# Optimization experiments

Hardware: AMD Instinct MI355X
Metric: run time of the kernel (lower is better)

Reference implementation:

```python
import jax, jax.numpy as jnp
import numpy as np

EMBED_DIM = 384


def setup_inputs() -> dict:
    key = jax.random.key(0)
    k1, k2, k3 = jax.random.split(key, 3)
    B, P, N, C = 32, 4, 1024, EMBED_DIM
    x = jax.random.normal(k1, (B, P, N, C), dtype=jnp.float32)
    # 1x1 Conv2D on channel-last == linear on last dim; kernel [Cin, Cout]
    w_qkv = jax.random.normal(k2, (C, 1 + 2 * C), dtype=jnp.float32) * (1.0 / np.sqrt(C))
    b_qkv = jnp.zeros((1 + 2 * C,), dtype=jnp.float32)
    w_proj = jax.random.normal(k3, (C, C), dtype=jnp.float32) * (1.0 / np.sqrt(C))
    b_proj = jnp.zeros((C,), dtype=jnp.float32)
    return {"x": x, "w_qkv": w_qkv, "b_qkv": b_qkv, "w_proj": w_proj, "b_proj": b_proj}


def reference(x, w_qkv, b_qkv, w_proj, b_proj):
    C = EMBED_DIM
    # qkv pointwise conv: [B,P,N,C] @ [C, 1+2C]
    qkv = jnp.einsum('bpnc,cd->bpnd', x, w_qkv) + b_qkv
    query = qkv[..., :1]                 # [B,P,N,1]
    key_t = qkv[..., 1:1 + C]            # [B,P,N,C]
    value = qkv[..., 1 + C:]             # [B,P,N,C]
    # NOTE: softmax over the trailing axis of size 1 (faithful to source) -> all ones
    context_scores = jax.nn.softmax(query, axis=-1)
    # key * scores, reduce-sum over patch-index axis (axis=2), keepdims
    context_vector = jnp.sum(key_t * context_scores, axis=2, keepdims=True)  # [B,P,1,C]
    gated = jax.nn.relu(value) * context_vector                              # [B,P,N,C]
    out = jnp.einsum('bpnc,cd->bpnd', gated, w_proj) + b_proj
    return out
```

## Files before the change

kernel.cpp:

```cpp
#include <hip/hip_runtime.h>
#include <hip/hip_bf16.h>
#include <type_traits>
#include <utility>

#define C_    384
#define N_    1024
#define G_    128
#define QKVD  769

typedef float  f32x4 __attribute__((ext_vector_type(4)));
typedef short  s16x8 __attribute__((ext_vector_type(8)));
typedef __bf16 b16x8 __attribute__((ext_vector_type(8)));

template <typename V, typename = void>
struct mfma_takes : std::false_type {};
template <typename V>
struct mfma_takes<V, std::void_t<decltype(__builtin_amdgcn_mfma_f32_16x16x32_bf16(
    std::declval<V>(), std::declval<V>(), std::declval<f32x4>(), 0, 0, 0))>>
    : std::true_type {};

using frag_t = std::conditional_t<mfma_takes<s16x8>::value, s16x8, b16x8>;

template <typename V>
__device__ __forceinline__ f32x4 mfma_bf16(V a, V b, f32x4 c) {
  return __builtin_amdgcn_mfma_f32_16x16x32_bf16(a, b, c, 0, 0, 0);
}

__device__ __forceinline__ unsigned short f2bf(float f) {
  union { float f; unsigned u; } v; v.f = f;
  unsigned r = v.u + 0x7fffu + ((v.u >> 16) & 1u);
  return (unsigned short)(r >> 16);
}
__device__ __forceinline__ unsigned pack2(float lo, float hi) {
  return (unsigned)f2bf(lo) | ((unsigned)f2bf(hi) << 16);
}

__global__ __launch_bounds__(384) void k_xsum(const float* __restrict__ x,
                                              float* __restrict__ xsum) {
  __shared__ float sh[4][C_];
  const int tid = threadIdx.x;
  const int c4  = (tid % 96) * 4;
  const int rg  = tid / 96;
  const int b   = blockIdx.x;
  const int g   = b >> 3;
  const float* p = x + ((size_t)b * 128 + (size_t)rg * 32) * C_ + c4;
  f32x4 s = {0.f, 0.f, 0.f, 0.f};
#pragma unroll 8
  for (int r = 0; r < 32; ++r) {
    float4 v = *(const float4*)(p + (size_t)r * C_);
    s.x += v.x; s.y += v.y; s.z += v.z; s.w += v.w;
  }
  *(f32x4*)&sh[rg][c4] = s;
  __syncthreads();
  if (rg == 0) {
#pragma unroll
    for (int j = 0; j < 4; ++j) {
      float v = sh[0][c4 + j] + sh[1][c4 + j] + sh[2][c4 + j] + sh[3][c4 + j];
      atomicAdd(&xsum[g * C_ + c4 + j], v);
    }
  }
}

__global__ void k_cv(const float* __restrict__ xsum, const float* __restrict__ w_qkv,
                     const float* __restrict__ b_qkv, float* __restrict__ cv) {
  __shared__ float xs[C_];
  int g = blockIdx.x, c = threadIdx.x;
  xs[c] = xsum[g * C_ + c];
  __syncthreads();
  float acc = 0.f;
#pragma unroll 4
  for (int k = 0; k < C_; ++k) acc += xs[k] * w_qkv[k * QKVD + 1 + c];
  cv[g * C_ + c] = acc + (float)N_ * b_qkv[1 + c];
}

__global__ void k_pack(const float* __restrict__ w_qkv, const float* __restrict__ w_proj,
                       unsigned short* __restrict__ pWv, unsigned short* __restrict__ pWp) {
  int bid = blockIdx.x;
  int mat = bid / 288;
  int r   = bid % 288;
  int kk = r / 24, nf = r % 24;
  int lane = threadIdx.x;
  int kbase = kk * 32 + (lane >> 4) * 8;
  int n = nf * 16 + (lane & 15);
  unsigned v[4];
#pragma unroll
  for (int jj = 0; jj < 4; ++jj) {
    int k0 = kbase + jj * 2;
    float f0 = mat ? w_proj[(size_t)k0 * C_ + n]       : w_qkv[(size_t)k0 * QKVD + 385 + n];
    float f1 = mat ? w_proj[(size_t)(k0 + 1) * C_ + n] : w_qkv[(size_t)(k0 + 1) * QKVD + 385 + n];
    v[jj] = (unsigned)f2bf(f0) | ((unsigned)f2bf(f1) << 16);
  }
  unsigned short* dst = (mat ? pWp : pWv) + ((size_t)r * 64 + lane) * 8;
  uint4 w; w.x = v[0]; w.y = v[1]; w.z = v[2]; w.w = v[3];
  *(uint4*)dst = w;
}

__global__ __launch_bounds__(256) void k_fused(
    const float* __restrict__ x, const unsigned short* __restrict__ pWv,
    const unsigned short* __restrict__ pWp, const float* __restrict__ cv,
    const float* __restrict__ b_qkv, const float* __restrict__ b_proj,
    float* __restrict__ out) {
  __shared__ __align__(16) char tile[32 * 768];
  __shared__ float cv_l[C_], bv_l[C_], bp_l[C_];

  const int tid  = threadIdx.x;
  const int lane = tid & 63;
  const int wv   = tid >> 6;
  const int R0   = blockIdx.x * 32;
  const int g    = R0 >> 10;

  for (int c = tid; c < C_; c += 256) {
    cv_l[c] = cv[g * C_ + c];
    bv_l[c] = b_qkv[1 + C_ + c];
    bp_l[c] = b_proj[c];
  }

  {
    const float* xg = x + (size_t)R0 * C_;
#pragma unroll
    for (int j = 0; j < 6; ++j) {
      int ch  = tid + j * 256;
      int row = ch / 48;
      int c8  = (ch % 48) * 8;
      const float4* s0 = (const float4*)(xg + (size_t)row * C_ + c8);
      float4 a = s0[0], b = s0[1];
      uint4 w;
      w.x = pack2(a.x, a.y); w.y = pack2(a.z, a.w);
      w.z = pack2(b.x, b.y); w.w = pack2(b.z, b.w);
      int byte = (row * 768 + c8 * 2) ^ ((row & 7) << 4);
      *(uint4*)(tile + byte) = w;
    }
  }
  __syncthreads();

  const f32x4 zero = {0.f, 0.f, 0.f, 0.f};
  f32x4 acc[2][6];
#pragma unroll
  for (int m = 0; m < 2; ++m)
#pragma unroll
    for (int n = 0; n < 6; ++n) acc[m][n] = zero;

  for (int kk = 0; kk < 12; ++kk) {
    frag_t A[2], Bv[6];
    int kb2 = (kk * 32 + (lane >> 4) * 8) * 2;
#pragma unroll
    for (int m = 0; m < 2; ++m) {
      int row = m * 16 + (lane & 15);
      A[m] = *(const frag_t*)(tile + ((row * 768 + kb2) ^ ((row & 7) << 4)));
    }
    const unsigned short* bp_ = pWv + ((size_t)(kk * 24 + wv * 6) * 64 + lane) * 8;
#pragma unroll
    for (int n = 0; n < 6; ++n) Bv[n] = *(const frag_t*)(bp_ + (size_t)n * 64 * 8);
#pragma unroll
    for (int m = 0; m < 2; ++m)
#pragma unroll
      for (int n = 0; n < 6; ++n) acc[m][n] = mfma_bf16(A[m], Bv[n], acc[m][n]);
  }
  __syncthreads();

#pragma unroll
  for (int m = 0; m < 2; ++m) {
#pragma unroll
    for (int n = 0; n < 6; ++n) {
      int col = wv * 96 + n * 16 + (lane & 15);
      float cvv = cv_l[col], bvv = bv_l[col];
#pragma unroll
      for (int r = 0; r < 4; ++r) {
        int row = m * 16 + (lane >> 4) * 4 + r;
        float val = fmaxf(acc[m][n][r] + bvv, 0.f) * cvv;
        *(unsigned short*)(tile + ((row * 768 + col * 2) ^ ((row & 7) << 4))) = f2bf(val);
      }
    }
  }
  __syncthreads();

#pragma unroll
  for (int m = 0; m < 2; ++m)
#pragma unroll
    for (int n = 0; n < 6; ++n) acc[m][n] = zero;

  for (int kk = 0; kk < 12; ++kk) {
    frag_t A[2], Bv[6];
    int kb2 = (kk * 32 + (lane >> 4) * 8) * 2;
#pragma unroll
    for (int m = 0; m < 2; ++m) {
      int row = m * 16 + (lane & 15);
      A[m] = *(const frag_t*)(tile + ((row * 768 + kb2) ^ ((row & 7) << 4)));
    }
    const unsigned short* bp_ = pWp + ((size_t)(kk * 24 + wv * 6) * 64 + lane) * 8;
#pragma unroll
    for (int n = 0; n < 6; ++n) Bv[n] = *(const frag_t*)(bp_ + (size_t)n * 64 * 8);
#pragma unroll
    for (int m = 0; m < 2; ++m)
#pragma unroll
      for (int n = 0; n < 6; ++n) acc[m][n] = mfma_bf16(A[m], Bv[n], acc[m][n]);
  }

#pragma unroll
  for (int m = 0; m < 2; ++m) {
#pragma unroll
    for (int n = 0; n < 6; ++n) {
      int col = wv * 96 + n * 16 + (lane & 15);
      float bpv = bp_l[col];
#pragma unroll
      for (int r = 0; r < 4; ++r) {
        int row = m * 16 + (lane >> 4) * 4 + r;
        out[(size_t)(R0 + row) * C_ + col] = acc[m][n][r] + bpv;
      }
    }
  }
}

extern "C" void kernel_launch(void* const* d_in, const int* in_sizes, int n_in,
                              void* d_out, int out_size, void* d_ws, size_t ws_size,
                              hipStream_t stream) {
  const float* x      = (const float*)d_in[0];
  const float* w_qkv  = (const float*)d_in[1];
  const float* b_qkv  = (const float*)d_in[2];
  const float* w_proj = (const float*)d_in[3];
  const float* b_proj = (const float*)d_in[4];
  float* out = (float*)d_out;

  float* xsum = (float*)d_ws;
  float* cvp  = xsum + G_ * C_;
  unsigned short* pWv = (unsigned short*)(cvp + G_ * C_);
  unsigned short* pWp = pWv + C_ * C_;

  hipMemsetAsync(xsum, 0, G_ * C_ * sizeof(float), stream);
  k_xsum<<<1024, 384, 0, stream>>>(x, xsum);
  k_pack<<<576, 64, 0, stream>>>(w_qkv, w_proj, pWv, pWp);
  k_cv<<<G_, C_, 0, stream>>>(xsum, w_qkv, b_qkv, cvp);
  k_fused<<<4096, 256, 0, stream>>>(x, pWv, pWp, cvp, b_qkv, b_proj, out);
}
```

Baseline: 228.9 us.

## Fuse column-sum into value GEMM and split into value/out kernels via bf16 workspace

Result: slower. 264.1 us (+15.4%).

```diff
diff --git a/kernel.cpp b/kernel.cpp
--- a/kernel.cpp
+++ b/kernel.cpp
@@ -7,6 +7,7 @@
 #define N_    1024
 #define G_    128
 #define QKVD  769
+#define TILEB 49152
 
 typedef float  f32x4 __attribute__((ext_vector_type(4)));
 typedef short  s16x8 __attribute__((ext_vector_type(8)));
@@ -34,31 +35,9 @@
 __device__ __forceinline__ unsigned pack2(float lo, float hi) {
   return (unsigned)f2bf(lo) | ((unsigned)f2bf(hi) << 16);
 }
-
-__global__ __launch_bounds__(384) void k_xsum(const float* __restrict__ x,
-                                              float* __restrict__ xsum) {
-  __shared__ float sh[4][C_];
-  const int tid = threadIdx.x;
-  const int c4  = (tid % 96) * 4;
-  const int rg  = tid / 96;
-  const int b   = blockIdx.x;
-  const int g   = b >> 3;
-  const float* p = x + ((size_t)b * 128 + (size_t)rg * 32) * C_ + c4;
-  f32x4 s = {0.f, 0.f, 0.f, 0.f};
-#pragma unroll 8
-  for (int r = 0; r < 32; ++r) {
-    float4 v = *(const float4*)(p + (size_t)r * C_);
-    s.x += v.x; s.y += v.y; s.z += v.z; s.w += v.w;
-  }
-  *(f32x4*)&sh[rg][c4] = s;
-  __syncthreads();
-  if (rg == 0) {
-#pragma unroll
-    for (int j = 0; j < 4; ++j) {
-      float v = sh[0][c4 + j] + sh[1][c4 + j] + sh[2][c4 + j] + sh[3][c4 + j];
-      atomicAdd(&xsum[g * C_ + c4 + j], v);
-    }
-  }
+__device__ __forceinline__ float bf2f(unsigned short b) {
+  union { unsigned u; float f; } v; v.u = (unsigned)b << 16;
+  return v.f;
 }
 
 __global__ void k_cv(const float* __restrict__ xsum, const float* __restrict__ w_qkv,
@@ -95,44 +74,52 @@
   *(uint4*)dst = w;
 }
 
-__global__ __launch_bounds__(256) void k_fused(
+__global__ __launch_bounds__(512) void k_val(
     const float* __restrict__ x, const unsigned short* __restrict__ pWv,
-    const unsigned short* __restrict__ pWp, const float* __restrict__ cv,
-    const float* __restrict__ b_qkv, const float* __restrict__ b_proj,
-    float* __restrict__ out) {
-  __shared__ __align__(16) char tile[32 * 768];
-  __shared__ float cv_l[C_], bv_l[C_], bp_l[C_];
+    const float* __restrict__ b_qkv, char* __restrict__ vws,
+    float* __restrict__ xsum) {
+  __shared__ __align__(16) char tile[TILEB];
+  __shared__ float csum[C_], bv_l[C_];
 
   const int tid  = threadIdx.x;
   const int lane = tid & 63;
   const int wv   = tid >> 6;
-  const int R0   = blockIdx.x * 32;
+  const int R0   = blockIdx.x * 64;
   const int g    = R0 >> 10;
 
-  for (int c = tid; c < C_; c += 256) {
-    cv_l[c] = cv[g * C_ + c];
+  for (int c = tid; c < C_; c += 512) {
+    csum[c] = 0.f;
     bv_l[c] = b_qkv[1 + C_ + c];
-    bp_l[c] = b_proj[c];
-  }
-
-  {
+  }
+  __syncthreads();
+
+  if (tid < 384) {
     const float* xg = x + (size_t)R0 * C_;
-#pragma unroll
-    for (int j = 0; j < 6; ++j) {
-      int ch  = tid + j * 256;
-      int row = ch / 48;
-      int c8  = (ch % 48) * 8;
-      const float4* s0 = (const float4*)(xg + (size_t)row * C_ + c8);
-      float4 a = s0[0], b = s0[1];
+    const int c8 = (tid % 48) * 8;
+    const int r0 = (tid / 48) * 8;
+    float s0=0,s1=0,s2=0,s3=0,s4=0,s5=0,s6=0,s7=0;
+#pragma unroll
+    for (int j = 0; j < 8; ++j) {
+      int row = r0 + j;
+      float4 a = *(const float4*)(xg + (size_t)row * C_ + c8);
+      float4 b = *(const float4*)(xg + (size_t)row * C_ + c8 + 4);
       uint4 w;
       w.x = pack2(a.x, a.y); w.y = pack2(a.z, a.w);
       w.z = pack2(b.x, b.y); w.w = pack2(b.z, b.w);
       int byte = (row * 768 + c8 * 2) ^ ((row & 7) << 4);
       *(uint4*)(tile + byte) = w;
-    }
-  }
-  __syncthreads();
-
+      s0 += a.x; s1 += a.y; s2 += a.z; s3 += a.w;
+      s4 += b.x; s5 += b.y; s6 += b.z; s7 += b.w;
+    }
+    atomicAdd(&csum[c8 + 0], s0); atomicAdd(&csum[c8 + 1], s1);
+    atomicAdd(&csum[c8 + 2], s2); atomicAdd(&csum[c8 + 3], s3);
+    atomicAdd(&csum[c8 + 4], s4); atomicAdd(&csum[c8 + 5], s5);
+    atomicAdd(&csum[c8 + 6], s6); atomicAdd(&csum[c8 + 7], s7);
+  }
+  __syncthreads();
+  if (tid < 384) atomicAdd(&xsum[g * C_ + tid], csum[tid]);
+
+  const int wr = wv >> 2, wc = wv & 3;
   const f32x4 zero = {0.f, 0.f, 0.f, 0.f};
   f32x4 acc[2][6];
 #pragma unroll
@@ -145,10 +132,10 @@
     int kb2 = (kk * 32 + (lane >> 4) * 8) * 2;
 #pragma unroll
     for (int m = 0; m < 2; ++m) {
-      int row = m * 16 + (lane & 15);
+      int row = wr * 32 + m * 16 + (lane & 15);
       A[m] = *(const frag_t*)(tile + ((row * 768 + kb2) ^ ((row & 7) << 4)));
     }
-    const unsigned short* bp_ = pWv + ((size_t)(kk * 24 + wv * 6) * 64 + lane) * 8;
+    const unsigned short* bp_ = pWv + ((size_t)(kk * 24 + wc * 6) * 64 + lane) * 8;
 #pragma unroll
     for (int n = 0; n < 6; ++n) Bv[n] = *(const frag_t*)(bp_ + (size_t)n * 64 * 8);
 #pragma unroll
@@ -162,18 +149,73 @@
   for (int m = 0; m < 2; ++m) {
 #pragma unroll
     for (int n = 0; n < 6; ++n) {
-      int col = wv * 96 + n * 16 + (lane & 15);
-      float cvv = cv_l[col], bvv = bv_l[col];
+      int col = wc * 96 + n * 16 + (lane & 15);
+      float bvv = bv_l[col];
 #pragma unroll
       for (int r = 0; r < 4; ++r) {
-        int row = m * 16 + (lane >> 4) * 4 + r;
-        float val = fmaxf(acc[m][n][r] + bvv, 0.f) * cvv;
+        int row = wr * 32 + m * 16 + (lane >> 4) * 4 + r;
+        float val = fmaxf(acc[m][n][r] + bvv, 0.f);
         *(unsigned short*)(tile + ((row * 768 + col * 2) ^ ((row & 7) << 4))) = f2bf(val);
       }
     }
   }
   __syncthreads();
 
+  const uint4* st = (const uint4*)tile;
+  uint4* dst = (uint4*)(vws + (size_t)blockIdx.x * TILEB);
+#pragma unroll
+  for (int j = 0; j < 6; ++j) {
+    int idx = tid + j * 512;
+    dst[idx] = st[idx];
+  }
+}
+
+__global__ __launch_bounds__(512) void k_out(
+    const char* __restrict__ vws, const unsigned short* __restrict__ pWp,
+    const float* __restrict__ cv, const float* __restrict__ b_proj,
+    float* __restrict__ out) {
+  __shared__ __align__(16) char tile[TILEB];
+  __shared__ float cv_l[C_], bp_l[C_];
+
+  const int tid  = threadIdx.x;
+  const int lane = tid & 63;
+  const int wv   = tid >> 6;
+  const int R0   = blockIdx.x * 64;
+  const int g    = R0 >> 10;
+
+  for (int c = tid; c < C_; c += 512) {
+    cv_l[c] = cv[g * C_ + c];
+    bp_l[c] = b_proj[c];
+  }
+  __syncthreads();
+
+  {
+    const uint4* src = (const uint4*)(vws + (size_t)blockIdx.x * TILEB);
+    uint4* dt = (uint4*)tile;
+#pragma unroll
+    for (int j = 0; j < 6; ++j) {
+      int idx = tid + j * 512;
+      int row = idx / 48;
+      int off = ((idx % 48) * 16) ^ ((row & 7) << 4);
+      int col0 = off >> 1;
+      uint4 w = src[idx];
+      unsigned d[4] = {w.x, w.y, w.z, w.w};
+      unsigned o[4];
+#pragma unroll
+      for (int q = 0; q < 4; ++q) {
+        float lo = bf2f((unsigned short)(d[q] & 0xffffu)) * cv_l[col0 + 2 * q];
+        float hi = bf2f((unsigned short)(d[q] >> 16))     * cv_l[col0 + 2 * q + 1];
+        o[q] = pack2(lo, hi);
+      }
+      uint4 ww; ww.x = o[0]; ww.y = o[1]; ww.z = o[2]; ww.w = o[3];
+      dt[idx] = ww;
+    }
+  }
+  __syncthreads();
+
+  const int wr = wv >> 2, wc = wv & 3;
+  const f32x4 zero = {0.f, 0.f, 0.f, 0.f};
+  f32x4 acc[2][6];
 #pragma unroll
   for (int m = 0; m < 2; ++m)
 #pragma unroll
@@ -184,10 +226,10 @@
     int kb2 = (kk * 32 + (lane >> 4) * 8) * 2;
 #pragma unroll
     for (int m = 0; m < 2; ++m) {
-      int row = m * 16 + (lane & 15);
+      int row = wr * 32 + m * 16 + (lane & 15);
       A[m] = *(const frag_t*)(tile + ((row * 768 + kb2) ^ ((row & 7) << 4)));
     }
-    const unsigned short* bp_ = pWp + ((size_t)(kk * 24 + wv * 6) * 64 + lane) * 8;
+    const unsigned short* bp_ = pWp + ((size_t)(kk * 24 + wc * 6) * 64 + lane) * 8;
 #pragma unroll
     for (int n = 0; n < 6; ++n) Bv[n] = *(const frag_t*)(bp_ + (size_t)n * 64 * 8);
 #pragma unroll
@@ -200,11 +242,11 @@
   for (int m = 0; m < 2; ++m) {
 #pragma unroll
     for (int n = 0; n < 6; ++n) {
-      int col = wv * 96 + n * 16 + (lane & 15);
+      int col = wc * 96 + n * 16 + (lane & 15);
       float bpv = bp_l[col];
 #pragma unroll
       for (int r = 0; r < 4; ++r) {
-        int row = m * 16 + (lane >> 4) * 4 + r;
+        int row = wr * 32 + m * 16 + (lane >> 4) * 4 + r;
         out[(size_t)(R0 + row) * C_ + col] = acc[m][n][r] + bpv;
       }
     }
@@ -225,10 +267,11 @@
   float* cvp  = xsum + G_ * C_;
   unsigned short* pWv = (unsigned short*)(cvp + G_ * C_);
   unsigned short* pWp = pWv + C_ * C_;
+  char* vws = (char*)(pWp + C_ * C_);
 
   hipMemsetAsync(xsum, 0, G_ * C_ * sizeof(float), stream);
-  k_xsum<<<1024, 384, 0, stream>>>(x, xsum);
   k_pack<<<576, 64, 0, stream>>>(w_qkv, w_proj, pWv, pWp);
+  k_val<<<2048, 512, 0, stream>>>(x, pWv, b_qkv, vws, xsum);
   k_cv<<<G_, C_, 0, stream>>>(xsum, w_qkv, b_qkv, cvp);
-  k_fused<<<4096, 256, 0, stream>>>(x, pWv, pWp, cvp, b_qkv, b_proj, out);
-}
+  k_out<<<2048, 512, 0, stream>>>(vws, pWp, cvp, b_proj, out);
+}
```

## Fuse xsum, context vector and GEMMs into one cooperative persistent kernel

Applied to the files above, without the earlier changes.

Measured after the change: 878.4 us. +283.7%, slower.

```diff
diff --git a/kernel.cpp b/kernel.cpp
--- a/kernel.cpp
+++ b/kernel.cpp
@@ -1,12 +1,17 @@
 #include <hip/hip_runtime.h>
+#include <hip/hip_cooperative_groups.h>
 #include <hip/hip_bf16.h>
 #include <type_traits>
 #include <utility>
 
-#define C_    384
-#define N_    1024
-#define G_    128
-#define QKVD  769
+#define C_     384
+#define N_     1024
+#define G_     128
+#define QKVD   769
+#define NBLK   512
+#define TILE_B 24576
+
+namespace cg = cooperative_groups;
 
 typedef float  f32x4 __attribute__((ext_vector_type(4)));
 typedef short  s16x8 __attribute__((ext_vector_type(8)));
@@ -33,6 +38,206 @@
 }
 __device__ __forceinline__ unsigned pack2(float lo, float hi) {
   return (unsigned)f2bf(lo) | ((unsigned)f2bf(hi) << 16);
+}
+
+__device__ __forceinline__ void stage16(const char* g, char* lbase, int lane) {
+#if __has_builtin(__builtin_amdgcn_global_load_lds)
+  __builtin_amdgcn_global_load_lds(
+      (const __attribute__((address_space(1))) void*)g,
+      (__attribute__((address_space(3))) void*)lbase, 16, 0, 0);
+#else
+  *(uint4*)(lbase + lane * 16) = *(const uint4*)g;
+#endif
+}
+
+__global__ void k_pack(const float* __restrict__ w_qkv, const float* __restrict__ w_proj,
+                       unsigned short* __restrict__ pWv, unsigned short* __restrict__ pWp) {
+  int bid = blockIdx.x;
+  int mat = bid / 288;
+  int r   = bid % 288;
+  int kk = r / 24, nf = r % 24;
+  int lane = threadIdx.x;
+  int kbase = kk * 32 + (lane >> 4) * 8;
+  int n = nf * 16 + (lane & 15);
+  unsigned v[4];
+#pragma unroll
+  for (int jj = 0; jj < 4; ++jj) {
+    int k0 = kbase + jj * 2;
+    float f0 = mat ? w_proj[(size_t)k0 * C_ + n]       : w_qkv[(size_t)k0 * QKVD + 385 + n];
+    float f1 = mat ? w_proj[(size_t)(k0 + 1) * C_ + n] : w_qkv[(size_t)(k0 + 1) * QKVD + 385 + n];
+    v[jj] = (unsigned)f2bf(f0) | ((unsigned)f2bf(f1) << 16);
+  }
+  unsigned short* dst = (mat ? pWp : pWv) + ((size_t)r * 64 + lane) * 8;
+  uint4 w; w.x = v[0]; w.y = v[1]; w.z = v[2]; w.w = v[3];
+  *(uint4*)dst = w;
+}
+
+__global__ __launch_bounds__(512, 4) void k_coop(
+    const float* __restrict__ x, const float* __restrict__ w_qkv,
+    const float* __restrict__ b_qkv, const float* __restrict__ b_proj,
+    const unsigned short* __restrict__ pWv, const unsigned short* __restrict__ pWp,
+    float* __restrict__ xsum, float* __restrict__ cvp,
+    char* __restrict__ xbb, float* __restrict__ out) {
+  __shared__ __align__(16) char buf[2][TILE_B];
+  __shared__ float xs[C_];
+
+  const int tid  = threadIdx.x;
+  const int lane = tid & 63;
+  const int wv   = tid >> 6;
+  const int b    = blockIdx.x;
+  const int g    = b >> 2;
+
+  if (tid < 384) {
+    const int col8 = (tid % 48) * 8;
+    const int rgrp = tid / 48;
+    float s0=0,s1=0,s2=0,s3=0,s4=0,s5=0,s6=0,s7=0;
+    for (int t = 0; t < 8; ++t) {
+      const float* xt = x + ((size_t)b * 256 + (size_t)t * 32) * C_;
+      char* img = xbb + (size_t)(b * 8 + t) * TILE_B;
+#pragma unroll
+      for (int jj = 0; jj < 4; ++jj) {
+        int row = rgrp * 4 + jj;
+        float4 a = *(const float4*)(xt + (size_t)row * C_ + col8);
+        float4 c = *(const float4*)(xt + (size_t)row * C_ + col8 + 4);
+        uint4 w;
+        w.x = pack2(a.x, a.y); w.y = pack2(a.z, a.w);
+        w.z = pack2(c.x, c.y); w.w = pack2(c.z, c.w);
+        *(uint4*)(img + ((row * 768 + col8 * 2) ^ ((row & 7) << 4))) = w;
+        s0 += a.x; s1 += a.y; s2 += a.z; s3 += a.w;
+        s4 += c.x; s5 += c.y; s6 += c.z; s7 += c.w;
+      }
+    }
+    atomicAdd(&xsum[g * C_ + col8 + 0], s0);
+    atomicAdd(&xsum[g * C_ + col8 + 1], s1);
+    atomicAdd(&xsum[g * C_ + col8 + 2], s2);
+    atomicAdd(&xsum[g * C_ + col8 + 3], s3);
+    atomicAdd(&xsum[g * C_ + col8 + 4], s4);
+    atomicAdd(&xsum[g * C_ + col8 + 5], s5);
+    atomicAdd(&xsum[g * C_ + col8 + 6], s6);
+    atomicAdd(&xsum[g * C_ + col8 + 7], s7);
+  }
+
+  cg::this_grid().sync();
+
+  if (tid < C_) xs[tid] = xsum[g * C_ + tid];
+  __syncthreads();
+  if (tid < 96) {
+    int c = (b & 3) * 96 + tid;
+    float acc = 0.f;
+#pragma unroll 4
+    for (int k = 0; k < C_; ++k) acc += xs[k] * w_qkv[k * QKVD + 1 + c];
+    cvp[g * C_ + c] = acc + (float)N_ * b_qkv[1 + c];
+  }
+
+  cg::this_grid().sync();
+
+  float cvr[3], bvr[3], bpr[3];
+#pragma unroll
+  for (int n = 0; n < 3; ++n) {
+    int col = wv * 48 + n * 16 + (lane & 15);
+    cvr[n] = cvp[g * C_ + col];
+    bvr[n] = b_qkv[1 + C_ + col];
+    bpr[n] = b_proj[col];
+  }
+
+  const char* myxb = xbb + (size_t)b * 8 * TILE_B;
+  const f32x4 zero = {0.f, 0.f, 0.f, 0.f};
+
+#pragma unroll
+  for (int j = 0; j < 3; ++j) {
+    int cb = (wv * 3 + j) * 1024;
+    stage16(myxb + cb + lane * 16, (char*)buf[0] + cb, lane);
+  }
+  __syncthreads();
+
+#pragma unroll 1
+  for (int t = 0; t < 8; ++t) {
+    const int p = t & 1;
+
+    if (t < 7) {
+      const char* src = myxb + (size_t)(t + 1) * TILE_B;
+#pragma unroll
+      for (int j = 0; j < 3; ++j) {
+        int cb = (wv * 3 + j) * 1024;
+        stage16(src + cb + lane * 16, (char*)buf[p ^ 1] + cb, lane);
+      }
+    }
+
+    f32x4 acc[2][3];
+#pragma unroll
+    for (int m = 0; m < 2; ++m)
+#pragma unroll
+      for (int n = 0; n < 3; ++n) acc[m][n] = zero;
+
+    for (int kk = 0; kk < 12; ++kk) {
+      frag_t A[2], Bv[3];
+      int kb2 = (kk * 32 + (lane >> 4) * 8) * 2;
+#pragma unroll
+      for (int m = 0; m < 2; ++m) {
+        int row = m * 16 + (lane & 15);
+        A[m] = *(const frag_t*)(buf[p] + ((row * 768 + kb2) ^ ((row & 7) << 4)));
+      }
+      const unsigned short* bp_ = pWv + ((size_t)(kk * 24 + wv * 3) * 64 + lane) * 8;
+#pragma unroll
+      for (int n = 0; n < 3; ++n) Bv[n] = *(const frag_t*)(bp_ + (size_t)n * 64 * 8);
+#pragma unroll
+      for (int m = 0; m < 2; ++m)
+#pragma unroll
+        for (int n = 0; n < 3; ++n) acc[m][n] = mfma_bf16(A[m], Bv[n], acc[m][n]);
+    }
+    __syncthreads();
+
+#pragma unroll
+    for (int m = 0; m < 2; ++m) {
+#pragma unroll
+      for (int n = 0; n < 3; ++n) {
+        int col = wv * 48 + n * 16 + (lane & 15);
+#pragma unroll
+        for (int r = 0; r < 4; ++r) {
+          int row = m * 16 + (lane >> 4) * 4 + r;
+          float val = fmaxf(acc[m][n][r] + bvr[n], 0.f) * cvr[n];
+          *(unsigned short*)(buf[p] + ((row * 768 + col * 2) ^ ((row & 7) << 4))) = f2bf(val);
+        }
+      }
+    }
+    __syncthreads();
+
+#pragma unroll
+    for (int m = 0; m < 2; ++m)
+#pragma unroll
+      for (int n = 0; n < 3; ++n) acc[m][n] = zero;
+
+    for (int kk = 0; kk < 12; ++kk) {
+      frag_t A[2], Bv[3];
+      int kb2 = (kk * 32 + (lane >> 4) * 8) * 2;
+#pragma unroll
+      for (int m = 0; m < 2; ++m) {
+        int row = m * 16 + (lane & 15);
+        A[m] = *(const frag_t*)(buf[p] + ((row * 768 + kb2) ^ ((row & 7) << 4)));
+      }
+      const unsigned short* bp_ = pWp + ((size_t)(kk * 24 + wv * 3) * 64 + lane) * 8;
+#pragma unroll
+      for (int n = 0; n < 3; ++n) Bv[n] = *(const frag_t*)(bp_ + (size_t)n * 64 * 8);
+#pragma unroll
+      for (int m = 0; m < 2; ++m)
+#pragma unroll
+        for (int n = 0; n < 3; ++n) acc[m][n] = mfma_bf16(A[m], Bv[n], acc[m][n]);
+    }
+
+#pragma unroll
+    for (int m = 0; m < 2; ++m) {
+#pragma unroll
+      for (int n = 0; n < 3; ++n) {
+        int col = wv * 48 + n * 16 + (lane & 15);
+#pragma unroll
+        for (int r = 0; r < 4; ++r) {
+          int row = m * 16 + (lane >> 4) * 4 + r;
+          out[((size_t)b * 256 + (size_t)t * 32 + row) * C_ + col] = acc[m][n][r] + bpr[n];
+        }
+      }
+    }
+    __syncthreads();
+  }
 }
 
 __global__ __launch_bounds__(384) void k_xsum(const float* __restrict__ x,
@@ -73,28 +278,6 @@
   cv[g * C_ + c] = acc + (float)N_ * b_qkv[1 + c];
 }
 
-__global__ void k_pack(const float* __restrict__ w_qkv, const float* __restrict__ w_proj,
-                       unsigned short* __restrict__ pWv, unsigned short* __restrict__ pWp) {
-  int bid = blockIdx.x;
-  int mat = bid / 288;
-  int r   = bid % 288;
-  int kk = r / 24, nf = r % 24;
-  int lane = threadIdx.x;
-  int kbase = kk * 32 + (lane >> 4) * 8;
-  int n = nf * 16 + (lane & 15);
-  unsigned v[4];
-#pragma unroll
-  for (int jj = 0; jj < 4; ++jj) {
-    int k0 = kbase + jj * 2;
-    float f0 = mat ? w_proj[(size_t)k0 * C_ + n]       : w_qkv[(size_t)k0 * QKVD + 385 + n];
-    float f1 = mat ? w_proj[(size_t)(k0 + 1) * C_ + n] : w_qkv[(size_t)(k0 + 1) * QKVD + 385 + n];
-    v[jj] = (unsigned)f2bf(f0) | ((unsigned)f2bf(f1) << 16);
-  }
-  unsigned short* dst = (mat ? pWp : pWv) + ((size_t)r * 64 + lane) * 8;
-  uint4 w; w.x = v[0]; w.y = v[1]; w.z = v[2]; w.w = v[3];
-  *(uint4*)dst = w;
-}
-
 __global__ __launch_bounds__(256) void k_fused(
     const float* __restrict__ x, const unsigned short* __restrict__ pWv,
     const unsigned short* __restrict__ pWp, const float* __restrict__ cv,
@@ -114,7 +297,6 @@
     bv_l[c] = b_qkv[1 + C_ + c];
     bp_l[c] = b_proj[c];
   }
-
   {
     const float* xg = x + (size_t)R0 * C_;
 #pragma unroll
@@ -225,10 +407,25 @@
   float* cvp  = xsum + G_ * C_;
   unsigned short* pWv = (unsigned short*)(cvp + G_ * C_);
   unsigned short* pWp = pWv + C_ * C_;
+  char* xbb = (char*)(pWp + C_ * C_);
+
+  const size_t need = 983040 + (size_t)NBLK * 8 * TILE_B;
 
   hipMemsetAsync(xsum, 0, G_ * C_ * sizeof(float), stream);
-  k_xsum<<<1024, 384, 0, stream>>>(x, xsum);
   k_pack<<<576, 64, 0, stream>>>(w_qkv, w_proj, pWv, pWp);
-  k_cv<<<G_, C_, 0, stream>>>(xsum, w_qkv, b_qkv, cvp);
-  k_fused<<<4096, 256, 0, stream>>>(x, pWv, pWp, cvp, b_qkv, b_proj, out);
-}
+
+  bool coop_ok = false;
+  if (ws_size >= need) {
+    void* args[10] = {(void*)&x, (void*)&w_qkv, (void*)&b_qkv, (void*)&b_proj,
+                      (void*)&pWv, (void*)&pWp, (void*)&xsum, (void*)&cvp,
+                      (void*)&xbb, (void*)&out};
+    hipError_t e = hipLaunchCooperativeKernel((const void*)k_coop, dim3(NBLK),
+                                              dim3(512), args, 0, stream);
+    coop_ok = (e == hipSuccess);
+  }
+  if (!coop_ok) {
+    k_xsum<<<1024, 384, 0, stream>>>(x, xsum);
+    k_cv<<<G_, C_, 0, stream>>>(xsum, w_qkv, b_qkv, cvp);
+    k_fused<<<4096, 256, 0, stream>>>(x, pWv, pWp, cvp, b_qkv, b_proj, out);
+  }
+}
```
